# Optimization experiments

Hardware: AMD Instinct MI355X
Metric: run time of the kernel (lower is better)

Reference implementation:

```python
import jax, jax.numpy as jnp
import numpy as np

D_IN = 768
D_SAE = 768 * 16  # expansion_factor = 16
K = 64
BATCH = 8192


def setup_inputs() -> dict:
    key = jax.random.key(0)
    k1, k2, k3 = jax.random.split(key, 3)
    x = jax.random.normal(k1, (BATCH, D_IN), dtype=jnp.float32)
    # Kaiming-uniform-ish encoder init (exact init values don't matter for correctness)
    bound = (6.0 / D_IN) ** 0.5
    W_enc = jax.random.uniform(k2, (D_IN, D_SAE), dtype=jnp.float32, minval=-bound, maxval=bound)
    b_enc = jnp.zeros((D_SAE,), dtype=jnp.float32)
    W_dec = jax.random.normal(k3, (D_SAE, D_IN), dtype=jnp.float32) * (1.0 / D_IN ** 0.5)
    # unit-norm decoder rows (per the module's normalize_decoder_weights)
    W_dec = W_dec / (jnp.linalg.norm(W_dec, axis=1, keepdims=True) + 1e-8)
    b_dec = jnp.zeros((D_IN,), dtype=jnp.float32)
    return {"x": x, "W_enc": W_enc, "b_enc": b_enc, "W_dec": W_dec, "b_dec": b_dec}


def reference(x, W_enc, b_enc, W_dec, b_dec):
    # encode: center, dense matmul, ReLU
    pre_acts = jax.nn.relu((x - b_dec) @ W_enc + b_enc)  # [B, d_sae]
    # top-k selection per row, scatter back into dense sparse_acts
    topk_vals, topk_idx = jax.lax.top_k(pre_acts, K)  # [B, K]
    rows = jnp.arange(pre_acts.shape[0])[:, None]  # [B, 1]
    sparse_acts = jnp.zeros_like(pre_acts).at[rows, topk_idx].set(topk_vals)
    # decode: dense matmul + bias
    reconstruction = sparse_acts @ W_dec + b_dec  # [B, d_in]
    return (reconstruction, sparse_acts)
```

## Files before the change

### kernel.cpp

```cpp
#include <hip/hip_runtime.h>
#include <hip/hip_fp16.h>
#include <stdint.h>

#define D_IN   768
#define D_SAE  12288
#define BATCH  8192
#define K_TOP  64
#define CAND_MAX 256

typedef _Float16 f16;
typedef _Float16 v8h __attribute__((ext_vector_type(8)));
typedef float v4f __attribute__((ext_vector_type(4)));

__device__ inline void async16(const void* g, void* l) {
    __builtin_amdgcn_global_load_lds(
        (const __attribute__((address_space(1))) unsigned int*)g,
        (__attribute__((address_space(3))) unsigned int*)l, 16, 0, 0);
}

__global__ __launch_bounds__(256) void k_convert_x(
    const float* __restrict__ x, const float* __restrict__ b_dec,
    f16* __restrict__ xhi, f16* __restrict__ xlo)
{
    int i4 = (blockIdx.x * 256 + threadIdx.x) * 4;
    float4 v = *(const float4*)(x + i4);
    int col = i4 % D_IN;
    float vv[4] = { v.x - b_dec[col], v.y - b_dec[col + 1],
                    v.z - b_dec[col + 2], v.w - b_dec[col + 3] };
    union { short4 s; f16 h[4]; } H, L;
#pragma unroll
    for (int u = 0; u < 4; ++u) {
        H.h[u] = (f16)vv[u];
        L.h[u] = (f16)(vv[u] - (float)H.h[u]);
    }
    *(short4*)(xhi + i4) = H.s;
    *(short4*)(xlo + i4) = L.s;
}

__global__ __launch_bounds__(256) void k_convert_wt(
    const float* __restrict__ W, f16* __restrict__ whiT, f16* __restrict__ wloT)
{
    __shared__ float tile[32][33];
    const int n0 = blockIdx.x * 32;
    const int k0 = blockIdx.y * 32;
    const int c = threadIdx.x & 31;
    const int rr = threadIdx.x >> 5;
#pragma unroll
    for (int s = 0; s < 4; ++s) {
        int r = s * 8 + rr;
        tile[r][c] = W[(size_t)(k0 + r) * D_SAE + n0 + c];
    }
    __syncthreads();
#pragma unroll
    for (int s = 0; s < 4; ++s) {
        int r2 = s * 8 + rr;
        float v = tile[c][r2];
        f16 hi = (f16)v;
        f16 lo = (f16)(v - (float)hi);
        whiT[(size_t)(n0 + r2) * D_IN + k0 + c] = hi;
        wloT[(size_t)(n0 + r2) * D_IN + k0 + c] = lo;
    }
}

__global__ __launch_bounds__(256) void k_gemm_f16(
    const f16* __restrict__ A,
    const f16* __restrict__ Bt,
    const float* __restrict__ b_enc,
    f16* __restrict__ outap)
{
    __shared__ f16 Asm[2][128 * 32];
    __shared__ f16 Bsm[2][128 * 32];
    const int tid  = threadIdx.x;
    const int wave = tid >> 6;
    const int lane = tid & 63;
    const int bn = blockIdx.x * 128;
    const int bm = blockIdx.y * 128;

    const int r16  = lane >> 2;
    const int kc8  = (lane & 3) * 8;
    const int mrow = lane & 15;
    const int quad = lane >> 4;
    const int wm = (wave & 1) * 64;
    const int wn = (wave >> 1) * 64;

    v4f acc[4][4] = {};

    const f16* gA = A  + (size_t)(bm + wave * 32 + r16) * D_IN + kc8;
    const f16* gB = Bt + (size_t)(bn + wave * 32 + r16) * D_IN + kc8;
    f16* lA0  = &Asm[0][(wave * 32) * 32];
    f16* lA0b = &Asm[0][(wave * 32 + 16) * 32];
    f16* lB0  = &Bsm[0][(wave * 32) * 32];
    f16* lB0b = &Bsm[0][(wave * 32 + 16) * 32];
    f16* lA1  = &Asm[1][(wave * 32) * 32];
    f16* lA1b = &Asm[1][(wave * 32 + 16) * 32];
    f16* lB1  = &Bsm[1][(wave * 32) * 32];
    f16* lB1b = &Bsm[1][(wave * 32 + 16) * 32];

    for (int k0 = 0; k0 < D_IN; k0 += 64) {
        __syncthreads();
        async16(gA + k0,               lA0);
        async16(gA + k0 + 16 * D_IN,   lA0b);
        async16(gB + k0,               lB0);
        async16(gB + k0 + 16 * D_IN,   lB0b);
        async16(gA + k0 + 32,              lA1);
        async16(gA + k0 + 32 + 16 * D_IN,  lA1b);
        async16(gB + k0 + 32,              lB1);
        async16(gB + k0 + 32 + 16 * D_IN,  lB1b);
        __syncthreads();

#pragma unroll
        for (int s = 0; s < 2; ++s) {
            v8h af[4], bf[4];
#pragma unroll
            for (int i = 0; i < 4; ++i)
                af[i] = *(const v8h*)&Asm[s][(wm + i * 16 + mrow) * 32 + quad * 8];
#pragma unroll
            for (int j = 0; j < 4; ++j)
                bf[j] = *(const v8h*)&Bsm[s][(wn + j * 16 + mrow) * 32 + quad * 8];
#pragma unroll
            for (int i = 0; i < 4; ++i)
#pragma unroll
                for (int j = 0; j < 4; ++j)
                    acc[i][j] = __builtin_amdgcn_mfma_f32_16x16x32_f16(af[i], bf[j], acc[i][j], 0, 0, 0);
        }
    }

#pragma unroll
    for (int i = 0; i < 4; ++i) {
#pragma unroll
        for (int r = 0; r < 4; ++r) {
            int grow = bm + wm + i * 16 + quad * 4 + r;
            f16* op = outap + (size_t)grow * (2 * D_SAE) + bn + wn;
#pragma unroll
            for (int j = 0; j < 4; ++j) {
                int c = j * 16 + mrow;
                float val = acc[i][j][r] + b_enc[bn + wn + c];
                __builtin_nontemporal_store((f16)(val > 0.f ? val : 0.f), op + c);
            }
        }
    }
}

__device__ __forceinline__ unsigned suffix_scan_256(unsigned h, int t, unsigned* wtot, unsigned* tot_out) {
    const int lane = t & 63;
    const int w = t >> 6;
    unsigned s = h;
#pragma unroll
    for (int off = 1; off < 64; off <<= 1) {
        unsigned o = __shfl_down(s, off);
        if (lane + off < 64) s += o;
    }
    if (lane == 0) wtot[w] = s;
    __syncthreads();
    unsigned suf = s;
    unsigned tot = 0;
#pragma unroll
    for (int w2 = 0; w2 < 4; ++w2) {
        tot += wtot[w2];
        if (w2 > w) suf += wtot[w2];
    }
    *tot_out = tot;
    return suf;
}

__global__ __launch_bounds__(256) void k_topk2(
    float* __restrict__ sparse,
    const f16* __restrict__ Xhi, const f16* __restrict__ Xlo,
    const f16* __restrict__ WhiT, const f16* __restrict__ WloT,
    const float* __restrict__ b_enc,
    const float* __restrict__ Wdec,
    const float* __restrict__ b_dec,
    float* __restrict__ recon)
{
    const int row = blockIdx.x;
    const int t = threadIdx.x;
    const int lane = t & 63;
    float* rp = sparse + (size_t)row * D_SAE;
    const f16* ap = (const f16*)rp;

    v8h av[6];
#pragma unroll
    for (int j = 0; j < 6; ++j)
        av[j] = __builtin_nontemporal_load((const v8h*)(ap + ((size_t)j * 256 + t) * 8));

    asm volatile("s_waitcnt vmcnt(0)" ::: "memory");
#pragma unroll
    for (int j = 0; j < 12; ++j) {
        v4f z = {0.f, 0.f, 0.f, 0.f};
        __builtin_nontemporal_store(z, (v4f*)(rp + ((size_t)j * 256 + t) * 4));
    }

    __shared__ unsigned hist[256];
    __shared__ unsigned wtot[4];
    __shared__ float sh_cutoff;
    __shared__ int sh_ncand;
    __shared__ int   cand_i[CAND_MAX];
    __shared__ float cand_v[CAND_MAX];
    __shared__ float kept_v[K_TOP];
    __shared__ int   kept_i[K_TOP];
    __shared__ float xr[D_IN];

    const float margin = 0.05f;

    hist[t] = 0;
    if (t == 0) sh_ncand = 0;
    for (int k = t; k < D_IN; k += 256)
        xr[k] = (float)Xhi[(size_t)row * D_IN + k] + (float)Xlo[(size_t)row * D_IN + k];
    __syncthreads();

#pragma unroll
    for (int j = 0; j < 6; ++j)
#pragma unroll
        for (int u = 0; u < 8; ++u) {
            float x = (float)av[j][u];
            if (x >= 2.0f) {
                int b = (int)((x - 2.0f) * 32.0f); if (b > 255) b = 255;
                atomicAdd(&hist[b], 1u);
            }
        }
    __syncthreads();
    unsigned h0 = hist[t];
    unsigned tot0;
    unsigned suf0 = suffix_scan_256(h0, t, wtot, &tot0);
    if (tot0 >= K_TOP) {
        if (suf0 >= K_TOP && suf0 - h0 < K_TOP)
            sh_cutoff = fmaxf(2.0f + (float)t * (1.0f / 32.0f) - margin, 1e-30f);
    }
    __syncthreads();
    if (tot0 < K_TOP) {
        hist[t] = 0;
        __syncthreads();
#pragma unroll
        for (int j = 0; j < 6; ++j)
#pragma unroll
            for (int u = 0; u < 8; ++u) {
                float x = (float)av[j][u];
                if (x >= 0.25f) {
                    int b = (int)(x * 32.0f); if (b > 255) b = 255;
                    atomicAdd(&hist[b], 1u);
                }
            }
        __syncthreads();
        unsigned h1 = hist[t];
        unsigned tot1;
        unsigned suf1 = suffix_scan_256(h1, t, wtot, &tot1);
        if (tot1 >= K_TOP) {
            if (suf1 >= K_TOP && suf1 - h1 < K_TOP)
                sh_cutoff = fmaxf((float)t * (1.0f / 32.0f) - margin, 1e-30f);
        }
        __syncthreads();
        if (tot1 < K_TOP) {
            hist[t] = 0;
            __syncthreads();
#pragma unroll
            for (int j = 0; j < 6; ++j)
#pragma unroll
                for (int u = 0; u < 8; ++u) {
                    float x = (float)av[j][u];
                    if (x > 0.0f && x < 0.25f) {
                        int b = (int)(x * 1024.0f); if (b > 255) b = 255;
                        atomicAdd(&hist[b], 1u);
                    }
                }
            __syncthreads();
            unsigned h2 = hist[t];
            unsigned tot2;
            unsigned suf2 = suffix_scan_256(h2, t, wtot, &tot2);
            unsigned need = K_TOP - tot1;
            if (tot2 >= need) {
                if (suf2 >= need && suf2 - h2 < need)
                    sh_cutoff = fmaxf((float)t * (1.0f / 1024.0f) - margin, 1e-30f);
            } else {
                if (t == 0) sh_cutoff = 1e-30f;
            }
        }
    }
    __syncthreads();
    const float cutoff = sh_cutoff;

#pragma unroll
    for (int j = 0; j < 6; ++j)
#pragma unroll
        for (int u = 0; u < 8; ++u) {
            float x = (float)av[j][u];
            bool pass = (x >= cutoff);
            unsigned long long m = __ballot(pass);
            if (m != 0ull) {
                int leader = (int)__builtin_ctzll(m);
                int cnt = (int)__builtin_popcountll(m);
                int base0 = 0;
                if (lane == leader) base0 = atomicAdd(&sh_ncand, cnt);
                base0 = __shfl(base0, leader);
                if (pass) {
                    int pos = base0 + (int)__builtin_popcountll(m & ((1ull << lane) - 1ull));
                    if (pos < CAND_MAX) { cand_i[pos] = (j * 256 + t) * 8 + u; cand_v[pos] = x; }
                }
            }
        }
    __syncthreads();
    int ncand = sh_ncand; if (ncand > CAND_MAX) ncand = CAND_MAX;

    for (int c = t; c < ncand; c += 256) {
        const f16* wh = WhiT + (size_t)cand_i[c] * D_IN;
        const f16* wl = WloT + (size_t)cand_i[c] * D_IN;
        float acc = 0.f;
        for (int k = 0; k < D_IN; k += 8) {
            v8h hv = *(const v8h*)(wh + k);
            v8h lv = *(const v8h*)(wl + k);
#pragma unroll
            for (int u = 0; u < 8; ++u)
                acc += xr[k + u] * ((float)hv[u] + (float)lv[u]);
        }
        acc += b_enc[cand_i[c]];
        cand_v[c] = acc > 0.f ? acc : 0.f;
    }
    __syncthreads();

    for (int c = t; c < ncand; c += 256) {
        float vc = cand_v[c]; int ic = cand_i[c];
        int r = 0;
        for (int m = 0; m < ncand; ++m) {
            float vm = cand_v[m];
            r += (vm > vc || (vm == vc && cand_i[m] < ic)) ? 1 : 0;
        }
        if (r < K_TOP) { kept_v[r] = vc; kept_i[r] = ic; }
    }
    __syncthreads();
    int nk = ncand < K_TOP ? ncand : K_TOP;

    if (t < nk) rp[kept_i[t]] = kept_v[t];

    float r0 = b_dec[t], r1 = b_dec[t + 256], r2 = b_dec[t + 512];
#pragma unroll 4
    for (int m = 0; m < nk; ++m) {
        float val = kept_v[m];
        const float* wr = Wdec + (size_t)kept_i[m] * D_IN;
        r0 += val * wr[t];
        r1 += val * wr[t + 256];
        r2 += val * wr[t + 512];
    }
    float* rc = recon + (size_t)row * D_IN;
    __builtin_nontemporal_store(r0, rc + t);
    __builtin_nontemporal_store(r1, rc + t + 256);
    __builtin_nontemporal_store(r2, rc + t + 512);
}

extern "C" void kernel_launch(void* const* d_in, const int* in_sizes, int n_in,
                              void* d_out, int out_size, void* d_ws, size_t ws_size,
                              hipStream_t stream) {
    const float* x     = (const float*)d_in[0];
    const float* W_enc = (const float*)d_in[1];
    const float* b_enc = (const float*)d_in[2];
    const float* W_dec = (const float*)d_in[3];
    const float* b_dec = (const float*)d_in[4];
    float* out    = (float*)d_out;
    float* recon  = out;
    float* sparse = out + (size_t)BATCH * D_IN;

    const size_t xplane = (size_t)BATCH * D_IN;
    const size_t wplane = (size_t)D_SAE * D_IN;
    f16* xhi  = (f16*)d_ws;
    f16* xlo  = xhi + xplane;
    f16* whiT = xlo + xplane;
    f16* wloT = whiT + wplane;

    k_convert_x<<<xplane / 1024, 256, 0, stream>>>(x, b_dec, xhi, xlo);
    k_convert_wt<<<dim3(D_SAE / 32, D_IN / 32), 256, 0, stream>>>(W_enc, whiT, wloT);
    k_gemm_f16<<<dim3(D_SAE / 128, BATCH / 128), 256, 0, stream>>>(xhi, whiT, b_enc, (f16*)sparse);
    k_topk2<<<BATCH, 256, 0, stream>>>(sparse, xhi, xlo, whiT, wloT, b_enc, W_dec, b_dec, recon);
}
```

Baseline: 1.245 ms.

## Pipeline GEMM K-loop, drop x low plane, use fp16 decoder, defer zeroing

After: 1.210 ms. 1.03x faster.

```diff
diff --git a/kernel.cpp b/kernel.cpp
--- a/kernel.cpp
+++ b/kernel.cpp
@@ -20,21 +20,17 @@
 
 __global__ __launch_bounds__(256) void k_convert_x(
     const float* __restrict__ x, const float* __restrict__ b_dec,
-    f16* __restrict__ xhi, f16* __restrict__ xlo)
+    f16* __restrict__ xhi)
 {
     int i4 = (blockIdx.x * 256 + threadIdx.x) * 4;
     float4 v = *(const float4*)(x + i4);
     int col = i4 % D_IN;
     float vv[4] = { v.x - b_dec[col], v.y - b_dec[col + 1],
                     v.z - b_dec[col + 2], v.w - b_dec[col + 3] };
-    union { short4 s; f16 h[4]; } H, L;
-#pragma unroll
-    for (int u = 0; u < 4; ++u) {
-        H.h[u] = (f16)vv[u];
-        L.h[u] = (f16)(vv[u] - (float)H.h[u]);
-    }
+    union { short4 s; f16 h[4]; } H;
+#pragma unroll
+    for (int u = 0; u < 4; ++u) H.h[u] = (f16)vv[u];
     *(short4*)(xhi + i4) = H.s;
-    *(short4*)(xlo + i4) = L.s;
 }
 
 __global__ __launch_bounds__(256) void k_convert_wt(
@@ -62,6 +58,16 @@
     }
 }
 
+__global__ __launch_bounds__(256) void k_convert_wd(
+    const float* __restrict__ W, f16* __restrict__ Wh)
+{
+    int i4 = (blockIdx.x * 256 + threadIdx.x) * 4;
+    float4 v = *(const float4*)(W + i4);
+    union { short4 s; f16 h[4]; } H;
+    H.h[0] = (f16)v.x; H.h[1] = (f16)v.y; H.h[2] = (f16)v.z; H.h[3] = (f16)v.w;
+    *(short4*)(Wh + i4) = H.s;
+}
+
 __global__ __launch_bounds__(256) void k_gemm_f16(
     const f16* __restrict__ A,
     const f16* __restrict__ Bt,
@@ -87,43 +93,37 @@
 
     const f16* gA = A  + (size_t)(bm + wave * 32 + r16) * D_IN + kc8;
     const f16* gB = Bt + (size_t)(bn + wave * 32 + r16) * D_IN + kc8;
-    f16* lA0  = &Asm[0][(wave * 32) * 32];
-    f16* lA0b = &Asm[0][(wave * 32 + 16) * 32];
-    f16* lB0  = &Bsm[0][(wave * 32) * 32];
-    f16* lB0b = &Bsm[0][(wave * 32 + 16) * 32];
-    f16* lA1  = &Asm[1][(wave * 32) * 32];
-    f16* lA1b = &Asm[1][(wave * 32 + 16) * 32];
-    f16* lB1  = &Bsm[1][(wave * 32) * 32];
-    f16* lB1b = &Bsm[1][(wave * 32 + 16) * 32];
-
-    for (int k0 = 0; k0 < D_IN; k0 += 64) {
+    f16* lA[2] = { &Asm[0][(wave * 32) * 32], &Asm[1][(wave * 32) * 32] };
+    f16* lB[2] = { &Bsm[0][(wave * 32) * 32], &Bsm[1][(wave * 32) * 32] };
+
+    #define STAGE(b, kk)                                   \
+        do {                                               \
+            async16(gA + (kk),            lA[b]);          \
+            async16(gA + (kk) + 16*D_IN,  lA[b] + 16*32);  \
+            async16(gB + (kk),            lB[b]);          \
+            async16(gB + (kk) + 16*D_IN,  lB[b] + 16*32);  \
+        } while (0)
+
+    STAGE(0, 0);
+#pragma unroll 2
+    for (int it = 0; it < 24; ++it) {
+        const int cur = it & 1;
         __syncthreads();
-        async16(gA + k0,               lA0);
-        async16(gA + k0 + 16 * D_IN,   lA0b);
-        async16(gB + k0,               lB0);
-        async16(gB + k0 + 16 * D_IN,   lB0b);
-        async16(gA + k0 + 32,              lA1);
-        async16(gA + k0 + 32 + 16 * D_IN,  lA1b);
-        async16(gB + k0 + 32,              lB1);
-        async16(gB + k0 + 32 + 16 * D_IN,  lB1b);
-        __syncthreads();
-
-#pragma unroll
-        for (int s = 0; s < 2; ++s) {
-            v8h af[4], bf[4];
-#pragma unroll
-            for (int i = 0; i < 4; ++i)
-                af[i] = *(const v8h*)&Asm[s][(wm + i * 16 + mrow) * 32 + quad * 8];
+        if (it + 1 < 24) STAGE(cur ^ 1, (it + 1) * 32);
+        v8h af[4], bf[4];
+#pragma unroll
+        for (int i = 0; i < 4; ++i)
+            af[i] = *(const v8h*)&Asm[cur][(wm + i * 16 + mrow) * 32 + quad * 8];
+#pragma unroll
+        for (int j = 0; j < 4; ++j)
+            bf[j] = *(const v8h*)&Bsm[cur][(wn + j * 16 + mrow) * 32 + quad * 8];
+#pragma unroll
+        for (int i = 0; i < 4; ++i)
 #pragma unroll
             for (int j = 0; j < 4; ++j)
-                bf[j] = *(const v8h*)&Bsm[s][(wn + j * 16 + mrow) * 32 + quad * 8];
-#pragma unroll
-            for (int i = 0; i < 4; ++i)
-#pragma unroll
-                for (int j = 0; j < 4; ++j)
-                    acc[i][j] = __builtin_amdgcn_mfma_f32_16x16x32_f16(af[i], bf[j], acc[i][j], 0, 0, 0);
-        }
-    }
+                acc[i][j] = __builtin_amdgcn_mfma_f32_16x16x32_f16(af[i], bf[j], acc[i][j], 0, 0, 0);
+    }
+    #undef STAGE
 
 #pragma unroll
     for (int i = 0; i < 4; ++i) {
@@ -165,10 +165,10 @@
 
 __global__ __launch_bounds__(256) void k_topk2(
     float* __restrict__ sparse,
-    const f16* __restrict__ Xhi, const f16* __restrict__ Xlo,
+    const float* __restrict__ x,
     const f16* __restrict__ WhiT, const f16* __restrict__ WloT,
     const float* __restrict__ b_enc,
-    const float* __restrict__ Wdec,
+    const f16* __restrict__ Wdh,
     const float* __restrict__ b_dec,
     float* __restrict__ recon)
 {
@@ -182,13 +182,6 @@
 #pragma unroll
     for (int j = 0; j < 6; ++j)
         av[j] = __builtin_nontemporal_load((const v8h*)(ap + ((size_t)j * 256 + t) * 8));
-
-    asm volatile("s_waitcnt vmcnt(0)" ::: "memory");
-#pragma unroll
-    for (int j = 0; j < 12; ++j) {
-        v4f z = {0.f, 0.f, 0.f, 0.f};
-        __builtin_nontemporal_store(z, (v4f*)(rp + ((size_t)j * 256 + t) * 4));
-    }
 
     __shared__ unsigned hist[256];
     __shared__ unsigned wtot[4];
@@ -205,16 +198,16 @@
     hist[t] = 0;
     if (t == 0) sh_ncand = 0;
     for (int k = t; k < D_IN; k += 256)
-        xr[k] = (float)Xhi[(size_t)row * D_IN + k] + (float)Xlo[(size_t)row * D_IN + k];
+        xr[k] = x[(size_t)row * D_IN + k] - b_dec[k];
     __syncthreads();
 
 #pragma unroll
     for (int j = 0; j < 6; ++j)
 #pragma unroll
         for (int u = 0; u < 8; ++u) {
-            float x = (float)av[j][u];
-            if (x >= 2.0f) {
-                int b = (int)((x - 2.0f) * 32.0f); if (b > 255) b = 255;
+            float x0 = (float)av[j][u];
+            if (x0 >= 2.0f) {
+                int b = (int)((x0 - 2.0f) * 32.0f); if (b > 255) b = 255;
                 atomicAdd(&hist[b], 1u);
             }
         }
@@ -234,9 +227,9 @@
         for (int j = 0; j < 6; ++j)
 #pragma unroll
             for (int u = 0; u < 8; ++u) {
-                float x = (float)av[j][u];
-                if (x >= 0.25f) {
-                    int b = (int)(x * 32.0f); if (b > 255) b = 255;
+                float x0 = (float)av[j][u];
+                if (x0 >= 0.25f) {
+                    int b = (int)(x0 * 32.0f); if (b > 255) b = 255;
                     atomicAdd(&hist[b], 1u);
                 }
             }
@@ -256,9 +249,9 @@
             for (int j = 0; j < 6; ++j)
 #pragma unroll
                 for (int u = 0; u < 8; ++u) {
-                    float x = (float)av[j][u];
-                    if (x > 0.0f && x < 0.25f) {
-                        int b = (int)(x * 1024.0f); if (b > 255) b = 255;
+                    float x0 = (float)av[j][u];
+                    if (x0 > 0.0f && x0 < 0.25f) {
+                        int b = (int)(x0 * 1024.0f); if (b > 255) b = 255;
                         atomicAdd(&hist[b], 1u);
                     }
                 }
@@ -282,8 +275,8 @@
     for (int j = 0; j < 6; ++j)
 #pragma unroll
         for (int u = 0; u < 8; ++u) {
-            float x = (float)av[j][u];
-            bool pass = (x >= cutoff);
+            float x0 = (float)av[j][u];
+            bool pass = (x0 >= cutoff);
             unsigned long long m = __ballot(pass);
             if (m != 0ull) {
                 int leader = (int)__builtin_ctzll(m);
@@ -293,7 +286,7 @@
                 base0 = __shfl(base0, leader);
                 if (pass) {
                     int pos = base0 + (int)__builtin_popcountll(m & ((1ull << lane) - 1ull));
-                    if (pos < CAND_MAX) { cand_i[pos] = (j * 256 + t) * 8 + u; cand_v[pos] = x; }
+                    if (pos < CAND_MAX) { cand_i[pos] = (j * 256 + t) * 8 + u; cand_v[pos] = x0; }
                 }
             }
         }
@@ -328,16 +321,22 @@
     __syncthreads();
     int nk = ncand < K_TOP ? ncand : K_TOP;
 
+#pragma unroll
+    for (int j = 0; j < 12; ++j) {
+        v4f z = {0.f, 0.f, 0.f, 0.f};
+        __builtin_nontemporal_store(z, (v4f*)(rp + ((size_t)j * 256 + t) * 4));
+    }
+    __syncthreads();
     if (t < nk) rp[kept_i[t]] = kept_v[t];
 
     float r0 = b_dec[t], r1 = b_dec[t + 256], r2 = b_dec[t + 512];
 #pragma unroll 4
     for (int m = 0; m < nk; ++m) {
         float val = kept_v[m];
-        const float* wr = Wdec + (size_t)kept_i[m] * D_IN;
-        r0 += val * wr[t];
-        r1 += val * wr[t + 256];
-        r2 += val * wr[t + 512];
+        const f16* wr = Wdh + (size_t)kept_i[m] * D_IN;
+        r0 += val * (float)wr[t];
+        r1 += val * (float)wr[t + 256];
+        r2 += val * (float)wr[t + 512];
     }
     float* rc = recon + (size_t)row * D_IN;
     __builtin_nontemporal_store(r0, rc + t);
@@ -360,12 +359,13 @@
     const size_t xplane = (size_t)BATCH * D_IN;
     const size_t wplane = (size_t)D_SAE * D_IN;
     f16* xhi  = (f16*)d_ws;
-    f16* xlo  = xhi + xplane;
-    f16* whiT = xlo + xplane;
+    f16* whiT = xhi + xplane;
     f16* wloT = whiT + wplane;
-
-    k_convert_x<<<xplane / 1024, 256, 0, stream>>>(x, b_dec, xhi, xlo);
+    f16* wdh  = wloT + wplane;
+
+    k_convert_x<<<xplane / 1024, 256, 0, stream>>>(x, b_dec, xhi);
     k_convert_wt<<<dim3(D_SAE / 32, D_IN / 32), 256, 0, stream>>>(W_enc, whiT, wloT);
+    k_convert_wd<<<wplane / 1024, 256, 0, stream>>>(W_dec, wdh);
     k_gemm_f16<<<dim3(D_SAE / 128, BATCH / 128), 256, 0, stream>>>(xhi, whiT, b_enc, (f16*)sparse);
-    k_topk2<<<BATCH, 256, 0, stream>>>(sparse, xhi, xlo, whiT, wloT, b_enc, W_dec, b_dec, recon);
-}
+    k_topk2<<<BATCH, 256, 0, stream>>>(sparse, x, whiT, wloT, b_enc, wdh, b_dec, recon);
+}
```
